# Kernel optimization log

Hardware: AMD Instinct MI355X
Metric: run time of the kernel (lower is better)

## Reference

```python
import jax, jax.numpy as jnp
import numpy as np

N, E = 100000, 1600000
ENT, OCU, SAI, IJ = 64, 64, 64, 8


def setup_inputs() -> dict:
    key = jax.random.key(0)
    ks = jax.random.split(key, 14)

    def lin(k, fan_in, fan_out):
        s = 1.0 / np.sqrt(fan_in)
        kw, kb = jax.random.split(k)
        w = jax.random.uniform(kw, (fan_in, fan_out), minval=-s, maxval=s, dtype=jnp.float32)
        b = jax.random.uniform(kb, (fan_out,), minval=-s, maxval=s, dtype=jnp.float32)
        return w, b

    we_w1, we_b1 = lin(ks[0], 2 * ENT + 1 + IJ, OCU)
    we_w2, we_b2 = lin(ks[1], OCU, OCU)
    wx_w1, wx_b1 = lin(ks[2], OCU, OCU)
    wx_w2, wx_b2 = lin(ks[3], OCU, 1)
    wh_w1, wh_b1 = lin(ks[4], ENT + OCU, OCU)
    wh_w2, wh_b2 = lin(ks[5], OCU, SAI)
    wv_w1, wv_b1 = lin(ks[6], ENT, OCU)
    wv_w2, wv_b2 = lin(ks[7], OCU, 1)

    return {
        "h": jax.random.normal(ks[8], (N, ENT), dtype=jnp.float32),
        "x": jax.random.normal(ks[9], (N, 3), dtype=jnp.float32),
        "velocidade": jax.random.normal(ks[10], (N, 3), dtype=jnp.float32),
        "atributos_arestas": jax.random.normal(ks[11], (E, IJ), dtype=jnp.float32),
        "we_w1": we_w1, "we_b1": we_b1, "we_w2": we_w2, "we_b2": we_b2,
        "wx_w1": wx_w1, "wx_b1": wx_b1, "wx_w2": wx_w2, "wx_b2": wx_b2,
        "wh_w1": wh_w1, "wh_b1": wh_b1, "wh_w2": wh_w2, "wh_b2": wh_b2,
        "wv_w1": wv_w1, "wv_b1": wv_b1, "wv_w2": wv_w2, "wv_b2": wv_b2,
        "arestas": jax.random.randint(ks[12], (2, E), 0, N, dtype=jnp.int32),
    }


def reference(h, x, velocidade, atributos_arestas,
              we_w1, we_b1, we_w2, we_b2,
              wx_w1, wx_b1, wx_w2, wx_b2,
              wh_w1, wh_b1, wh_w2, wh_b2,
              wv_w1, wv_b1, wv_w2, wv_b2,
              arestas):
    linhas, cols = arestas[0], arestas[1]
    n = h.shape[0]

    # gather endpoint coordinates, radial distance per edge
    diferenca = x[linhas] - x[cols]                            # [E, 3]
    dif_radial = jnp.sum(diferenca * diferenca, axis=1, keepdims=True)  # [E, 1]

    # edge MLP phi_e on [h_i, h_j, ||x_i-x_j||^2, edge_attr]
    atributos = jnp.concatenate([h[linhas], h[cols], dif_radial, atributos_arestas], axis=1)
    m_ij = jnp.tanh(jnp.tanh(atributos @ we_w1 + we_b1) @ we_w2 + we_b2)   # [E, OCU]

    # phi_x: per-edge scalar gate on coordinate differences
    phi_x = jnp.tanh(jnp.tanh(m_ij @ wx_w1 + wx_b1) @ wx_w2 + wx_b2)       # [E, 1]

    # phi_v: per-node scalar gate on velocity
    phi_v = jnp.tanh(h @ wv_w1 + wv_b1) @ wv_w2 + wv_b2                    # [N, 1]

    # segment-mean of (diferenca * phi_x) over source nodes
    trans = diferenca * phi_x                                              # [E, 3]
    agg_sum = jax.ops.segment_sum(trans, linhas, num_segments=n)           # [N, 3]
    cnt = jax.ops.segment_sum(jnp.ones((E, 1), trans.dtype), linhas, num_segments=n)
    agg_mean = agg_sum / jnp.maximum(cnt, 1.0)

    velocidade_nova = velocidade * phi_v + agg_mean
    x_nova = x + velocidade_nova

    # segment-sum of edge messages, node update phi_h
    m_i = jax.ops.segment_sum(m_ij, linhas, num_segments=n)                # [N, OCU]
    h_cat = jnp.concatenate([h, m_i], axis=1)
    h_nova = jnp.tanh(h_cat @ wh_w1 + wh_b1) @ wh_w2 + wh_b2               # [N, SAI]

    return (h_nova, x_nova, velocidade_nova)
```

## Files before the change

### kernel.cpp

```cpp
#include <hip/hip_runtime.h>


typedef unsigned int uint;
typedef unsigned short u16;
typedef __attribute__((ext_vector_type(8))) short short8;
typedef __attribute__((ext_vector_type(4))) float f32x4;

#define UB_LO(u) __uint_as_float((u) << 16)
#define UB_HI(u) __uint_as_float((u) & 0xffff0000u)

__device__ __forceinline__ float fast_tanh(float x) {
    float e = __expf(2.0f * x);
    return 1.0f - 2.0f * __builtin_amdgcn_rcpf(e + 1.0f);
}
__device__ __forceinline__ u16 bf16rne(float f) {
    uint u = __float_as_uint(f);
    return (u16)((u + 0x7fffu + ((u >> 16) & 1u)) >> 16);
}
__device__ __forceinline__ uint packbf(float a, float b) {
    return (uint)bf16rne(a) | ((uint)bf16rne(b) << 16);
}
__device__ __forceinline__ uint packbf_fast(float a, float b) {
    return __builtin_amdgcn_perm(__float_as_uint(b), __float_as_uint(a), 0x07060302u);
}
__device__ __forceinline__ u16 trunc16(float f) {
    return (u16)(__float_as_uint(f) >> 16);
}
__device__ __forceinline__ int swzb(int b) { return b ^ ((b >> 3) & 0x70); }

__global__ void wprep_hist_kernel(const float* __restrict__ we_w1, const float* __restrict__ we_w2,
                                  const float* __restrict__ wx_w1, const float* __restrict__ wv_w1,
                                  const float* __restrict__ wh_w1, const float* __restrict__ wh_w2,
                                  u16* __restrict__ we1t, u16* __restrict__ we2t,
                                  u16* __restrict__ wx1t, u16* __restrict__ wv1t,
                                  u16* __restrict__ wh1t, u16* __restrict__ wh2t,
                                  u16* __restrict__ wert,
                                  const int* __restrict__ rows, int* __restrict__ hist, int E) {
    const int b = blockIdx.x;
    if (b < 32) {
        int t = b * 256 + threadIdx.x;
        if (t < 8192) {
            int j = t >> 7, k = t & 127;
            we1t[t] = bf16rne(we_w1[k * 64 + j]);
            wh1t[t] = bf16rne(wh_w1[k * 64 + j]);
        }
        if (t < 4096) {
            int n = t >> 6, k = t & 63;
            we2t[t] = bf16rne(we_w2[k * 64 + n]);
            wx1t[t] = bf16rne(wx_w1[k * 64 + n]);
            wv1t[t] = bf16rne(wv_w1[k * 64 + n]);
            wh2t[t] = bf16rne(wh_w2[k * 64 + n]);
        }
        if (t < 2048) {
            int n = t >> 5, k = t & 31;
            float v = 0.0f;
            if (k == 0) v = we_w1[128 * 64 + n];
            else if (k <= 8) v = we_w1[(128 + k) * 64 + n];
            wert[t] = bf16rne(v);
        }
    } else {
        int e = (b - 32) * 256 + threadIdx.x;
        if (e < E) atomicAdd(&hist[rows[e]], 1);
    }
}

__global__ __launch_bounds__(256, 4)
void pre_mfma_kernel(const float* __restrict__ h, const float* __restrict__ we_b1,
                     const u16* __restrict__ we1t,
                     u16* __restrict__ HrB, u16* __restrict__ HcB, int N)
{
    __shared__ u16 X1[4096];
    __shared__ u16 X2[4096];
    const int tid = threadIdx.x, lane = tid & 63, wv = tid >> 6;
    const int nb = blockIdx.x * 64;
    const int el = tid >> 2, jg = tid & 3;
    const int fn = lane & 15, fk8 = (lane >> 4) * 8;

    {
        uint pk[8];
        if (nb + el < N) {
            const float4* h4 = (const float4*)(h + (size_t)(nb + el) * 64 + jg * 16);
            #pragma unroll
            for (int q = 0; q < 4; q++) {
                float4 v = h4[q];
                pk[2*q]   = packbf_fast(v.x, v.y);
                pk[2*q+1] = packbf_fast(v.z, v.w);
            }
        } else {
            #pragma unroll
            for (int q = 0; q < 8; q++) pk[q] = 0;
        }
        const int b0 = swzb(el * 128 + jg * 32), b1 = swzb(el * 128 + jg * 32 + 16);
        *(uint4*)(&X1[b0 >> 1]) = make_uint4(pk[0], pk[1], pk[2], pk[3]);
        *(uint4*)(&X1[b1 >> 1]) = make_uint4(pk[4], pk[5], pk[6], pk[7]);
    }
    __syncthreads();

    const int mb = wv * 16;
    short8 a0, a1;
    {
        const int ba = swzb((mb + fn) * 128 + fk8 * 2);
        const int bb = swzb((mb + fn) * 128 + 64 + fk8 * 2);
        a0 = *(const short8*)(&X1[ba >> 1]);
        a1 = *(const short8*)(&X1[bb >> 1]);
    }
    #pragma unroll
    for (int n0 = 0; n0 < 4; n0++) {
        uint4 bw0 = *(const uint4*)(we1t + (n0*16 + fn) * 128 + fk8);
        uint4 bw1 = *(const uint4*)(we1t + (n0*16 + fn) * 128 + 32 + fk8);
        const float bias = we_b1[n0 * 16 + fn];
        f32x4 q = {bias, bias, bias, bias};
        q = __builtin_amdgcn_mfma_f32_16x16x32_bf16(a0, __builtin_bit_cast(short8, bw0), q, 0, 0, 0);
        q = __builtin_amdgcn_mfma_f32_16x16x32_bf16(a1, __builtin_bit_cast(short8, bw1), q, 0, 0, 0);
        #pragma unroll
        for (int r2 = 0; r2 < 4; r2++) {
            const int m = mb + (lane >> 4) * 4 + r2;
            X2[swzb(m * 128 + (n0*16 + fn) * 2) >> 1] = bf16rne(q[r2]);
        }
    }
    __syncthreads();
    if (nb + el < N) {
        const int b0 = swzb(el * 128 + jg * 32), b1 = swzb(el * 128 + jg * 32 + 16);
        uint4 v0 = *(const uint4*)(&X2[b0 >> 1]);
        uint4 v1 = *(const uint4*)(&X2[b1 >> 1]);
        u16* o = HrB + (size_t)(nb + el) * 64 + jg * 16;
        *(uint4*)o = v0; *(uint4*)(o + 8) = v1;
    }
    __syncthreads();
    #pragma unroll
    for (int n0 = 0; n0 < 4; n0++) {
        uint4 bw0 = *(const uint4*)(we1t + (n0*16 + fn) * 128 + 64 + fk8);
        uint4 bw1 = *(const uint4*)(we1t + (n0*16 + fn) * 128 + 96 + fk8);
        f32x4 q = {0.f, 0.f, 0.f, 0.f};
        q = __builtin_amdgcn_mfma_f32_16x16x32_bf16(a0, __builtin_bit_cast(short8, bw0), q, 0, 0, 0);
        q = __builtin_amdgcn_mfma_f32_16x16x32_bf16(a1, __builtin_bit_cast(short8, bw1), q, 0, 0, 0);
        #pragma unroll
        for (int r2 = 0; r2 < 4; r2++) {
            const int m = mb + (lane >> 4) * 4 + r2;
            X2[swzb(m * 128 + (n0*16 + fn) * 2) >> 1] = bf16rne(q[r2]);
        }
    }
    __syncthreads();
    if (nb + el < N) {
        const int b0 = swzb(el * 128 + jg * 32), b1 = swzb(el * 128 + jg * 32 + 16);
        uint4 v0 = *(const uint4*)(&X2[b0 >> 1]);
        uint4 v1 = *(const uint4*)(&X2[b1 >> 1]);
        u16* o = HcB + (size_t)(nb + el) * 64 + jg * 16;
        *(uint4*)o = v0; *(uint4*)(o + 8) = v1;
    }
}

__global__ __launch_bounds__(256, 8)
void edge_mfma_kernel(const float* __restrict__ x, const float* __restrict__ eattr,
                      const uint4* __restrict__ rec4,
                      const u16* __restrict__ HrB, const u16* __restrict__ HcB,
                      const u16* __restrict__ wert,
                      const u16* __restrict__ we2t, const float* __restrict__ we_b2,
                      const u16* __restrict__ wx1t, const float* __restrict__ wx_b1,
                      const float* __restrict__ wx_w2, const float* __restrict__ wx_b2,
                      float* __restrict__ miF, float* __restrict__ aggF,
                      float* __restrict__ cntF, int E)
{
    __shared__ u16 T[4096];
    __shared__ float dS[64][3];
    __shared__ float pxS[64];
    __shared__ float radS[64];
    __shared__ int rS[64];
    __shared__ int eS[64];

    const int tid = threadIdx.x, lane = tid & 63, wv = tid >> 6;
    int bid = blockIdx.x;
    const int nwg = gridDim.x;
    if ((nwg & 7) == 0) bid = (bid & 7) * (nwg >> 3) + (bid >> 3);
    const int sb = bid * 64;
    const int fn = lane & 15, fk8 = (lane >> 4) * 8;
    const int el = tid >> 2, jg = tid & 3;
    const int s = sb + el;
    const int mb = wv * 16;

    {
        int r = -1, c = 0;
        if (s < E) { uint4 p4 = rec4[s]; r = (int)p4.x; c = (int)p4.y;
                     if (jg == 0) eS[el] = (int)p4.z; }
        if (jg == 0) rS[el] = r;
        uint pk[8];
        if (s < E) {
            if (jg == 0) {
                const float d0 = x[(size_t)r*3+0] - x[(size_t)c*3+0];
                const float d1 = x[(size_t)r*3+1] - x[(size_t)c*3+1];
                const float d2 = x[(size_t)r*3+2] - x[(size_t)c*3+2];
                dS[el][0] = d0; dS[el][1] = d1; dS[el][2] = d2;
                radS[el] = d0*d0 + d1*d1 + d2*d2;
            }
            uint4 ra = *(const uint4*)(HrB + (size_t)r * 64 + jg * 16);
            uint4 rb = *(const uint4*)(HrB + (size_t)r * 64 + jg * 16 + 8);
            uint4 ca = *(const uint4*)(HcB + (size_t)c * 64 + jg * 16);
            uint4 cb = *(const uint4*)(HcB + (size_t)c * 64 + jg * 16 + 8);
            uint rw[8] = {ra.x, ra.y, ra.z, ra.w, rb.x, rb.y, rb.z, rb.w};
            uint cw[8] = {ca.x, ca.y, ca.z, ca.w, cb.x, cb.y, cb.z, cb.w};
            #pragma unroll
            for (int q = 0; q < 8; q++) {
                const float lo = UB_LO(rw[q]) + UB_LO(cw[q]);
                const float hi = UB_HI(rw[q]) + UB_HI(cw[q]);
                pk[q] = packbf_fast(lo, hi);
            }
        } else {
            #pragma unroll
            for (int q = 0; q < 8; q++) pk[q] = 0;
        }
        const int b0 = swzb(el * 128 + jg * 32), b1 = swzb(el * 128 + jg * 32 + 16);
        *(uint4*)(&T[b0 >> 1]) = make_uint4(pk[0], pk[1], pk[2], pk[3]);
        *(uint4*)(&T[b1 >> 1]) = make_uint4(pk[4], pk[5], pk[6], pk[7]);
    }
    __syncthreads();

    uint ae[4] = {0, 0, 0, 0};
    {
        const int kc = lane >> 4;
        const int s2 = sb + mb + fn;
        if (kc < 2 && s2 < E) {
            const int e2 = eS[mb + fn];
            const float4* ea4 = (const float4*)(eattr + (size_t)e2 * 8);
            if (kc == 0) {
                float4 u0 = ea4[0], u1 = ea4[1];
                const float rad = radS[mb + fn];
                ae[0] = packbf_fast(rad,  u0.x);
                ae[1] = packbf_fast(u0.y, u0.z);
                ae[2] = packbf_fast(u0.w, u1.x);
                ae[3] = packbf_fast(u1.y, u1.z);
            } else {
                float4 u1 = ea4[1];
                ae[0] = packbf_fast(u1.w, 0.0f);
            }
        }
    }
    const short8 a_e = __builtin_bit_cast(short8, *(uint4*)ae);

    #pragma unroll
    for (int n0 = 0; n0 < 4; n0++) {
        uint4 bw = *(const uint4*)(wert + (n0*16 + fn) * 32 + fk8);
        f32x4 q = {0.f, 0.f, 0.f, 0.f};
        q = __builtin_amdgcn_mfma_f32_16x16x32_bf16(a_e, __builtin_bit_cast(short8, bw), q, 0, 0, 0);
        #pragma unroll
        for (int r2 = 0; r2 < 4; r2++) {
            const int idx = swzb((mb + (lane >> 4) * 4 + r2) * 128 + (n0*16 + fn) * 2) >> 1;
            const float pre = q[r2] + UB_LO((uint)T[idx]);
            T[idx] = trunc16(fast_tanh(pre));
        }
    }

    short8 a0, a1;
    {
        const int ba = swzb((mb + fn) * 128 + fk8 * 2);
        const int bb = swzb((mb + fn) * 128 + 64 + fk8 * 2);
        a0 = *(const short8*)(&T[ba >> 1]);
        a1 = *(const short8*)(&T[bb >> 1]);
    }
    #pragma unroll
    for (int n0 = 0; n0 < 4; n0++) {
        uint4 bw0 = *(const uint4*)(we2t + (n0*16 + fn) * 64 + fk8);
        uint4 bw1 = *(const uint4*)(we2t + (n0*16 + fn) * 64 + 32 + fk8);
        const float bias = we_b2[n0 * 16 + fn];
        f32x4 q = {bias, bias, bias, bias};
        q = __builtin_amdgcn_mfma_f32_16x16x32_bf16(a0, __builtin_bit_cast(short8, bw0), q, 0, 0, 0);
        q = __builtin_amdgcn_mfma_f32_16x16x32_bf16(a1, __builtin_bit_cast(short8, bw1), q, 0, 0, 0);
        #pragma unroll
        for (int r2 = 0; r2 < 4; r2++) {
            const int m = mb + (lane >> 4) * 4 + r2;
            T[swzb(m * 128 + (n0*16 + fn) * 2) >> 1] = bf16rne(fast_tanh(q[r2]));
        }
    }

    short8 c0, c1;
    {
        const int ba = swzb((mb + fn) * 128 + fk8 * 2);
        const int bb = swzb((mb + fn) * 128 + 64 + fk8 * 2);
        c0 = *(const short8*)(&T[ba >> 1]);
        c1 = *(const short8*)(&T[bb >> 1]);
    }
    float pxp[4] = {0.f, 0.f, 0.f, 0.f};
    #pragma unroll
    for (int n0 = 0; n0 < 4; n0++) {
        uint4 bw0 = *(const uint4*)(wx1t + (n0*16 + fn) * 64 + fk8);
        uint4 bw1 = *(const uint4*)(wx1t + (n0*16 + fn) * 64 + 32 + fk8);
        const float bias = wx_b1[n0 * 16 + fn];
        f32x4 q = {bias, bias, bias, bias};
        q = __builtin_amdgcn_mfma_f32_16x16x32_bf16(c0, __builtin_bit_cast(short8, bw0), q, 0, 0, 0);
        q = __builtin_amdgcn_mfma_f32_16x16x32_bf16(c1, __builtin_bit_cast(short8, bw1), q, 0, 0, 0);
        const float wqn = wx_w2[n0 * 16 + fn];
        #pragma unroll
        for (int r2 = 0; r2 < 4; r2++) pxp[r2] += fast_tanh(q[r2]) * wqn;
    }
    #pragma unroll
    for (int off = 1; off < 16; off <<= 1) {
        #pragma unroll
        for (int r2 = 0; r2 < 4; r2++) pxp[r2] += __shfl_xor(pxp[r2], off, 64);
    }
    if (fn == 0) {
        const float bx2 = wx_b2[0];
        #pragma unroll
        for (int r2 = 0; r2 < 4; r2++) {
            const int m = mb + (lane >> 4) * 4 + r2;
            pxS[m] = fast_tanh(pxp[r2] + bx2);
        }
    }
    __syncthreads();

    {
        const int rl = rS[lane];
        const int rp = (lane > 0) ? rS[lane - 1] : -2;
        const unsigned long long startm = __ballot(lane == 0 || rl != rp);
        unsigned long long m = startm & (0xFFFFull << (wv * 16));
        while (m) {
            const int s0 = (int)__builtin_ctzll(m);
            m &= m - 1;
            const int r0 = rS[s0];
            if (r0 < 0) continue;
            const unsigned long long rest = (startm >> s0) >> 1;
            const int s1 = rest ? s0 + 1 + (int)__builtin_ctzll(rest) : 64;
            float msum = 0.0f, tsum = 0.0f;
            for (int t = s0; t < s1; t++) {
                msum += UB_LO((uint)T[swzb(t * 128 + lane * 2) >> 1]);
                if (lane < 3) tsum += dS[t][lane] * pxS[t];
            }
            atomicAdd(&miF[(size_t)r0 * 64 + lane], msum);
            if (lane < 3) atomicAdd(&aggF[(size_t)r0 * 3 + lane], tsum);
            if (lane == 3) atomicAdd(&cntF[r0], (float)(s1 - s0));
        }
    }
}

__global__ __launch_bounds__(256, 4)
void aggnode_kernel(const float* __restrict__ h, const float* __restrict__ x,
                    const float* __restrict__ vel,
                    const float* __restrict__ miF, const float* __restrict__ aggF,
                    const float* __restrict__ cntF,
                    const u16* __restrict__ wv1t, const float* __restrict__ wv_b1,
                    const float* __restrict__ wv_w2, const float* __restrict__ wv_b2,
                    const u16* __restrict__ wh1t, const float* __restrict__ wh_b1,
                    const u16* __restrict__ wh2t, const float* __restrict__ wh_b2,
                    float* __restrict__ out_h, float* __restrict__ out_x,
                    float* __restrict__ out_v, int N)
{
    __shared__ u16 Xh[4096];
    __shared__ u16 Xm[4096];
    __shared__ float aggM[64][3];
    __shared__ float pvS[64];

    const int tid = threadIdx.x, lane = tid & 63, wv = tid >> 6;
    const int nb = blockIdx.x * 64;
    const int el = tid >> 2, jg = tid & 3;
    const int fn = lane & 15, fk8 = (lane >> 4) * 8;

    {
        uint pk[8];
        if (nb + el < N) {
            const float4* h4 = (const float4*)(h + (size_t)(nb + el) * 64 + jg * 16);
            #pragma unroll
            for (int q = 0; q < 4; q++) {
                float4 v = h4[q];
                pk[2*q]   = packbf_fast(v.x, v.y);
                pk[2*q+1] = packbf_fast(v.z, v.w);
            }
        } else {
            #pragma unroll
            for (int q = 0; q < 8; q++) pk[q] = 0;
        }
        const int b0 = swzb(el * 128 + jg * 32), b1 = swzb(el * 128 + jg * 32 + 16);
        *(uint4*)(&Xh[b0 >> 1]) = make_uint4(pk[0], pk[1], pk[2], pk[3]);
        *(uint4*)(&Xh[b1 >> 1]) = make_uint4(pk[4], pk[5], pk[6], pk[7]);
    }

    for (int t = 0; t < 16; t++) {
        const int ln = wv * 16 + t;
        const int n = nb + ln;
        float val = 0.0f;
        if (n < N) val = miF[(size_t)n * 64 + lane];
        Xm[swzb(ln * 128 + lane * 2) >> 1] = bf16rne(val);
        if (lane < 3 && n < N) {
            const float cf = cntF[n];
            aggM[ln][lane] = aggF[(size_t)n * 3 + lane] / fmaxf(cf, 1.0f);
        }
    }
    __syncthreads();

    const int mb = wv * 16;
    short8 a0, a1, b0, b1;
    {
        const int ba = swzb((mb + fn) * 128 + fk8 * 2);
        const int bb = swzb((mb + fn) * 128 + 64 + fk8 * 2);
        a0 = *(const short8*)(&Xh[ba >> 1]);
        a1 = *(const short8*)(&Xh[bb >> 1]);
        b0 = *(const short8*)(&Xm[ba >> 1]);
        b1 = *(const short8*)(&Xm[bb >> 1]);
    }

    float pvp[4] = {0.f, 0.f, 0.f, 0.f};
    #pragma unroll
    for (int n0 = 0; n0 < 4; n0++) {
        uint4 bw0 = *(const uint4*)(wv1t + (n0*16 + fn) * 64 + fk8);
        uint4 bw1 = *(const uint4*)(wv1t + (n0*16 + fn) * 64 + 32 + fk8);
        const float bias = wv_b1[n0 * 16 + fn];
        f32x4 q = {bias, bias, bias, bias};
        q = __builtin_amdgcn_mfma_f32_16x16x32_bf16(a0, __builtin_bit_cast(short8, bw0), q, 0, 0, 0);
        q = __builtin_amdgcn_mfma_f32_16x16x32_bf16(a1, __builtin_bit_cast(short8, bw1), q, 0, 0, 0);
        const float wqn = wv_w2[n0 * 16 + fn];
        #pragma unroll
        for (int r2 = 0; r2 < 4; r2++) pvp[r2] += fast_tanh(q[r2]) * wqn;
    }
    #pragma unroll
    for (int off = 1; off < 16; off <<= 1) {
        #pragma unroll
        for (int r2 = 0; r2 < 4; r2++) pvp[r2] += __shfl_xor(pvp[r2], off, 64);
    }
    if (fn == 0) {
        const float bv2 = wv_b2[0];
        #pragma unroll
        for (int r2 = 0; r2 < 4; r2++) pvS[mb + (lane >> 4) * 4 + r2] = pvp[r2] + bv2;
    }
    __syncthreads();

    #pragma unroll
    for (int n0 = 0; n0 < 4; n0++) {
        const u16* base = wh1t + (n0*16 + fn) * 128;
        uint4 bw0 = *(const uint4*)(base + fk8);
        uint4 bw1 = *(const uint4*)(base + 32 + fk8);
        uint4 bw2 = *(const uint4*)(base + 64 + fk8);
        uint4 bw3 = *(const uint4*)(base + 96 + fk8);
        const float bias = wh_b1[n0 * 16 + fn];
        f32x4 q = {bias, bias, bias, bias};
        q = __builtin_amdgcn_mfma_f32_16x16x32_bf16(a0, __builtin_bit_cast(short8, bw0), q, 0, 0, 0);
        q = __builtin_amdgcn_mfma_f32_16x16x32_bf16(a1, __builtin_bit_cast(short8, bw1), q, 0, 0, 0);
        q = __builtin_amdgcn_mfma_f32_16x16x32_bf16(b0, __builtin_bit_cast(short8, bw2), q, 0, 0, 0);
        q = __builtin_amdgcn_mfma_f32_16x16x32_bf16(b1, __builtin_bit_cast(short8, bw3), q, 0, 0, 0);
        #pragma unroll
        for (int r2 = 0; r2 < 4; r2++) {
            const int m = mb + (lane >> 4) * 4 + r2;
            Xm[swzb(m * 128 + (n0*16 + fn) * 2) >> 1] = bf16rne(fast_tanh(q[r2]));
        }
    }
    __syncthreads();

    short8 c0, c1;
    {
        const int ba = swzb((mb + fn) * 128 + fk8 * 2);
        const int bb = swzb((mb + fn) * 128 + 64 + fk8 * 2);
        c0 = *(const short8*)(&Xm[ba >> 1]);
        c1 = *(const short8*)(&Xm[bb >> 1]);
    }
    #pragma unroll
    for (int n0 = 0; n0 < 4; n0++) {
        uint4 bw0 = *(const uint4*)(wh2t + (n0*16 + fn) * 64 + fk8);
        uint4 bw1 = *(const uint4*)(wh2t + (n0*16 + fn) * 64 + 32 + fk8);
        const float bias = wh_b2[n0 * 16 + fn];
        f32x4 q = {bias, bias, bias, bias};
        q = __builtin_amdgcn_mfma_f32_16x16x32_bf16(c0, __builtin_bit_cast(short8, bw0), q, 0, 0, 0);
        q = __builtin_amdgcn_mfma_f32_16x16x32_bf16(c1, __builtin_bit_cast(short8, bw1), q, 0, 0, 0);
        #pragma unroll
        for (int r2 = 0; r2 < 4; r2++) {
            const int m = mb + (lane >> 4) * 4 + r2;
            if (nb + m < N) out_h[(size_t)(nb + m) * 64 + n0 * 16 + fn] = q[r2];
        }
    }

    if (tid < 64 && nb + tid < N) {
        const int n = nb + tid;
        const float pv = pvS[tid];
        #pragma unroll
        for (int d = 0; d < 3; d++) {
            const float am = aggM[tid][d];
            const float vn = vel[(size_t)n * 3 + d] * pv + am;
            out_v[(size_t)n * 3 + d] = vn;
            out_x[(size_t)n * 3 + d] = x[(size_t)n * 3 + d] + vn;
        }
    }
}

__global__ __launch_bounds__(256)
void scan1_kernel(const int* __restrict__ hist, int* __restrict__ bsum, int N) {
    const int t = threadIdx.x, b = blockIdx.x;
    const int base = b * 1024 + t * 4;
    int s = 0;
    #pragma unroll
    for (int q = 0; q < 4; q++) s += (base + q < N) ? hist[base + q] : 0;
    #pragma unroll
    for (int off = 1; off < 64; off <<= 1) s += __shfl_xor(s, off, 64);
    __shared__ int ws[4];
    if ((t & 63) == 0) ws[t >> 6] = s;
    __syncthreads();
    if (t == 0) bsum[b] = ws[0] + ws[1] + ws[2] + ws[3];
}

__global__ __launch_bounds__(256)
void scan2_kernel(int* __restrict__ bsum, int nb) {
    __shared__ int buf[1024];
    const int t = threadIdx.x;
    for (int i = t; i < nb; i += 256) buf[i] = bsum[i];
    __syncthreads();
    if (t == 0) {
        int run = 0;
        for (int i = 0; i < nb; i++) { int v = buf[i]; buf[i] = run; run += v; }
    }
    __syncthreads();
    for (int i = t; i < nb; i += 256) bsum[i] = buf[i];
}

__global__ __launch_bounds__(256)
void scan3_kernel(const int* __restrict__ hist, const int* __restrict__ bbase,
                  int* __restrict__ offs, int* __restrict__ cursor, int N) {
    const int t = threadIdx.x, b = blockIdx.x;
    const int base = b * 1024 + t * 4;
    int v[4];
    #pragma unroll
    for (int q = 0; q < 4; q++) v[q] = (base + q < N) ? hist[base + q] : 0;
    const int s = v[0] + v[1] + v[2] + v[3];
    const int lane = t & 63, wid = t >> 6;
    int inc = s;
    #pragma unroll
    for (int off = 1; off < 64; off <<= 1) {
        int u = __shfl_up(inc, off, 64);
        if (lane >= off) inc += u;
    }
    __shared__ int wtot[4];
    if (lane == 63) wtot[wid] = inc;
    __syncthreads();
    int wbase = 0;
    #pragma unroll
    for (int wq = 0; wq < 3; wq++) if (wq < wid) wbase += wtot[wq];
    int run = bbase[b] + wbase + (inc - s);
    #pragma unroll
    for (int q = 0; q < 4; q++) {
        const int i = base + q;
        if (i < N) { cursor[i] = run; run += v[q]; offs[i + 1] = run; }
    }
    if (b == 0 && t == 0) offs[0] = 0;
}

__global__ void scatter_kernel(const int* __restrict__ rows, const int* __restrict__ cols,
                               int* __restrict__ cursor, uint4* __restrict__ rec4, int E) {
    int e = blockIdx.x * blockDim.x + threadIdx.x;
    if (e < E) {
        int r = rows[e];
        int p = atomicAdd(&cursor[r], 1);
        rec4[p] = make_uint4((uint)r, (uint)cols[e], (uint)e, 0u);
    }
}

template<int BLK>
__global__ __launch_bounds__(BLK)
void edge_atomic_kernel(const float* __restrict__ h, const float* __restrict__ x,
                 const float* __restrict__ eattr,
                 const int* __restrict__ rows, const int* __restrict__ cols,
                 const float* __restrict__ we_w1, const float* __restrict__ we_b1,
                 const float* __restrict__ we_w2, const float* __restrict__ we_b2,
                 const float* __restrict__ wx_w1, const float* __restrict__ wx_b1,
                 const float* __restrict__ wx_w2, const float* __restrict__ wx_b2,
                 float* __restrict__ agg, float* __restrict__ cnt, float* __restrict__ mi,
                 int E)
{
    __shared__ float act[64][BLK];
    const int tid = threadIdx.x;
    const int e = blockIdx.x * BLK + tid;
    if (e >= E) return;

    const int r = rows[e];
    const int c = cols[e];
    const float d0 = x[(size_t)r*3+0] - x[(size_t)c*3+0];
    const float d1 = x[(size_t)r*3+1] - x[(size_t)c*3+1];
    const float d2 = x[(size_t)r*3+2] - x[(size_t)c*3+2];
    const float rad = d0*d0 + d1*d1 + d2*d2;

    float A[64];
    #pragma unroll
    for (int j = 0; j < 64; j++) A[j] = we_b1[j];
    const float* hr = h + (size_t)r * 64;
    const float* hc = h + (size_t)c * 64;
    #pragma unroll 4
    for (int k = 0; k < 64; k++) {
        const float a0 = hr[k];
        const float a1 = hc[k];
        const float* w0 = we_w1 + k * 64;
        const float* w1 = we_w1 + (64 + k) * 64;
        #pragma unroll
        for (int j = 0; j < 64; j++) A[j] += a0 * w0[j] + a1 * w1[j];
    }
    {
        const float* w = we_w1 + 128 * 64;
        #pragma unroll
        for (int j = 0; j < 64; j++) A[j] += rad * w[j];
    }
    const float* ea = eattr + (size_t)e * 8;
    #pragma unroll
    for (int k = 0; k < 8; k++) {
        const float a = ea[k];
        const float* w = we_w1 + (129 + k) * 64;
        #pragma unroll
        for (int j = 0; j < 64; j++) A[j] += a * w[j];
    }
    #pragma unroll
    for (int j = 0; j < 64; j++) act[j][tid] = fast_tanh(A[j]);

    float B[64];
    #pragma unroll
    for (int j = 0; j < 64; j++) B[j] = we_b2[j];
    #pragma unroll 4
    for (int k = 0; k < 64; k++) {
        const float a = act[k][tid];
        const float* w = we_w2 + k * 64;
        #pragma unroll
        for (int j = 0; j < 64; j++) B[j] += a * w[j];
    }
    #pragma unroll
    for (int j = 0; j < 64; j++) act[j][tid] = fast_tanh(B[j]);

    #pragma unroll
    for (int j = 0; j < 64; j++) A[j] = wx_b1[j];
    #pragma unroll 4
    for (int k = 0; k < 64; k++) {
        const float a = act[k][tid];
        const float* w = wx_w1 + k * 64;
        #pragma unroll
        for (int j = 0; j < 64; j++) A[j] += a * w[j];
    }
    float px = wx_b2[0];
    #pragma unroll
    for (int j = 0; j < 64; j++) px += fast_tanh(A[j]) * wx_w2[j];
    px = fast_tanh(px);

    atomicAdd(&agg[(size_t)r*3+0], d0 * px);
    atomicAdd(&agg[(size_t)r*3+1], d1 * px);
    atomicAdd(&agg[(size_t)r*3+2], d2 * px);
    atomicAdd(&cnt[r], 1.0f);
    float* mir = mi + (size_t)r * 64;
    #pragma unroll
    for (int j = 0; j < 64; j++) atomicAdd(&mir[j], act[j][tid]);
}

template<int BLK>
__global__ __launch_bounds__(BLK, 2)
void node_fb_kernel(const float* __restrict__ h, const float* __restrict__ x,
                 const float* __restrict__ vel,
                 const float* __restrict__ wh_w1, const float* __restrict__ wh_b1,
                 const float* __restrict__ wh_w2, const float* __restrict__ wh_b2,
                 const float* __restrict__ wv_w1, const float* __restrict__ wv_b1,
                 const float* __restrict__ wv_w2, const float* __restrict__ wv_b2,
                 const float* __restrict__ agg, const float* __restrict__ cnt,
                 const float* __restrict__ mi,
                 float* __restrict__ out_h, float* __restrict__ out_x, float* __restrict__ out_v,
                 int N)
{
    const int n = blockIdx.x * BLK + threadIdx.x;
    if (n >= N) return;

    const float* hn = h + (size_t)n * 64;
    const float* mn = mi + (size_t)n * 64;

    float A[64];
    #pragma unroll
    for (int j = 0; j < 64; j++) A[j] = wv_b1[j];
    #pragma unroll
    for (int k = 0; k < 64; k++) {
        const float a = hn[k];
        const float* w = wv_w1 + k * 64;
        #pragma unroll
        for (int j = 0; j < 64; j++) A[j] += a * w[j];
    }
    float pv = wv_b2[0];
    #pragma unroll
    for (int j = 0; j < 64; j++) pv += fast_tanh(A[j]) * wv_w2[j];

    #pragma unroll
    for (int j = 0; j < 64; j++) A[j] = wh_b1[j];
    #pragma unroll
    for (int k = 0; k < 64; k++) {
        const float a0 = hn[k];
        const float a1 = mn[k];
        const float* w0 = wh_w1 + k * 64;
        const float* w1 = wh_w1 + (64 + k) * 64;
        #pragma unroll
        for (int j = 0; j < 64; j++) A[j] += a0 * w0[j] + a1 * w1[j];
    }
    #pragma unroll
    for (int j = 0; j < 64; j++) A[j] = fast_tanh(A[j]);

    float B[64];
    #pragma unroll
    for (int j = 0; j < 64; j++) B[j] = wh_b2[j];
    #pragma unroll
    for (int k = 0; k < 64; k++) {
        const float a = A[k];
        const float* w = wh_w2 + k * 64;
        #pragma unroll
        for (int j = 0; j < 64; j++) B[j] += a * w[j];
    }
    float* oh = out_h + (size_t)n * 64;
    #pragma unroll
    for (int j = 0; j < 64; j++) oh[j] = B[j];

    const float inv = 1.0f / fmaxf(cnt[n], 1.0f);
    #pragma unroll
    for (int d = 0; d < 3; d++) {
        const float am = agg[(size_t)n*3 + d] * inv;
        const float vn = vel[(size_t)n*3 + d] * pv + am;
        out_v[(size_t)n*3 + d] = vn;
        out_x[(size_t)n*3 + d] = x[(size_t)n*3 + d] + vn;
    }
}

extern "C" void kernel_launch(void* const* d_in, const int* in_sizes, int n_in,
                              void* d_out, int out_size, void* d_ws, size_t ws_size,
                              hipStream_t stream) {
    const float* h      = (const float*)d_in[0];
    const float* x      = (const float*)d_in[1];
    const float* vel    = (const float*)d_in[2];
    const float* eattr  = (const float*)d_in[3];
    const float* we_w1  = (const float*)d_in[4];
    const float* we_b1  = (const float*)d_in[5];
    const float* we_w2  = (const float*)d_in[6];
    const float* we_b2  = (const float*)d_in[7];
    const float* wx_w1  = (const float*)d_in[8];
    const float* wx_b1  = (const float*)d_in[9];
    const float* wx_w2  = (const float*)d_in[10];
    const float* wx_b2  = (const float*)d_in[11];
    const float* wh_w1  = (const float*)d_in[12];
    const float* wh_b1  = (const float*)d_in[13];
    const float* wh_w2  = (const float*)d_in[14];
    const float* wh_b2  = (const float*)d_in[15];
    const float* wv_w1  = (const float*)d_in[16];
    const float* wv_b1  = (const float*)d_in[17];
    const float* wv_w2  = (const float*)d_in[18];
    const float* wv_b2  = (const float*)d_in[19];
    const int*   ar     = (const int*)d_in[20];

    const int N = in_sizes[0] / 64;
    const int E = in_sizes[20] / 2;
    const int* rows = ar;
    const int* cols = ar + E;

    float* out_h = (float*)d_out;
    float* out_x = out_h + (size_t)N * 64;
    float* out_v = out_x + (size_t)N * 3;

    u16* HrB = (u16*)d_out;
    u16* HcB = HrB + (size_t)N * 64;

    const int nbScan = (N + 1023) / 1024;

    char* p = (char*)d_ws;
    float* miF  = (float*)p; p += (size_t)N * 64 * sizeof(float);
    float* aggF = (float*)p; p += (size_t)N * 3 * sizeof(float);
    float* cntF = (float*)p; p += (size_t)N * sizeof(float);
    int*  hist  = (int*)p;   p += (size_t)N * sizeof(int);
    const size_t zero_bytes = (size_t)(p - (char*)d_ws);
    int*  offs  = (int*)p;   p += (size_t)(N + 1) * sizeof(int);
    int*  cursor= (int*)p;   p += (size_t)N * sizeof(int);
    int*  bsum  = (int*)p;   p += (size_t)(nbScan > 0 ? nbScan : 1) * sizeof(int);
    p = (char*)(((uintptr_t)p + 15) & ~(uintptr_t)15);
    uint4* rec4 = (uint4*)p; p += (size_t)E * sizeof(uint4);
    p = (char*)(((uintptr_t)p + 63) & ~(uintptr_t)63);
    u16*  we1t = (u16*)p;   p += 64 * 128 * sizeof(u16);
    u16*  we2t = (u16*)p;   p += 64 * 64 * sizeof(u16);
    u16*  wx1t = (u16*)p;   p += 64 * 64 * sizeof(u16);
    u16*  wv1t = (u16*)p;   p += 64 * 64 * sizeof(u16);
    u16*  wh1t = (u16*)p;   p += 64 * 128 * sizeof(u16);
    u16*  wh2t = (u16*)p;   p += 64 * 64 * sizeof(u16);
    u16*  wert = (u16*)p;   p += 64 * 32 * sizeof(u16);
    const size_t needed = (size_t)(p - (char*)d_ws);

    if (ws_size >= needed && nbScan <= 1024) {
        hipMemsetAsync(d_ws, 0, zero_bytes, stream);
        wprep_hist_kernel<<<32 + (E + 255) / 256, 256, 0, stream>>>(
            we_w1, we_w2, wx_w1, wv_w1, wh_w1, wh_w2,
            we1t, we2t, wx1t, wv1t, wh1t, wh2t, wert, rows, hist, E);
        scan1_kernel<<<nbScan, 256, 0, stream>>>(hist, bsum, N);
        scan2_kernel<<<1, 256, 0, stream>>>(bsum, nbScan);
        scan3_kernel<<<nbScan, 256, 0, stream>>>(hist, bsum, offs, cursor, N);
        scatter_kernel<<<(E + 255) / 256, 256, 0, stream>>>(rows, cols, cursor, rec4, E);

        pre_mfma_kernel<<<(N + 63) / 64, 256, 0, stream>>>(h, we_b1, we1t, HrB, HcB, N);

        edge_mfma_kernel<<<(E + 63) / 64, 256, 0, stream>>>(
            x, eattr, rec4, HrB, HcB,
            wert, we2t, we_b2, wx1t, wx_b1, wx_w2, wx_b2,
            miF, aggF, cntF, E);

        aggnode_kernel<<<(N + 63) / 64, 256, 0, stream>>>(
            h, x, vel, miF, aggF, cntF,
            wv1t, wv_b1, wv_w2, wv_b2,
            wh1t, wh_b1, wh2t, wh_b2,
            out_h, out_x, out_v, N);
    } else {
        float* agg2 = (float*)d_ws;
        float* cnt2 = agg2 + (size_t)N * 3;
        float* mi2  = cnt2 + N;
        hipMemsetAsync(d_ws, 0, (size_t)N * 68 * sizeof(float), stream);

        edge_atomic_kernel<128><<<(E + 127) / 128, 128, 0, stream>>>(
            h, x, eattr, rows, cols,
            we_w1, we_b1, we_w2, we_b2,
            wx_w1, wx_b1, wx_w2, wx_b2,
            agg2, cnt2, mi2, E);

        node_fb_kernel<128><<<(N + 127) / 128, 128, 0, stream>>>(
            h, x, vel,
            wh_w1, wh_b1, wh_w2, wh_b2,
            wv_w1, wv_b1, wv_w2, wv_b2,
            agg2, cnt2, mi2, out_h, out_x, out_v, N);
    }
}
```

Before: 555.8 us.

## Make edge kernel persistent with register prefetch of next tile's gathers

The edge kernel now launches a fixed grid of up to 2048 blocks, and each block walks a contiguous range of 64-edge tiles. While the current tile runs its MFMA chain, the block loads the next tile's sorted edge record, coordinate differences and bf16 node-feature rows into registers. This overlaps gather latency with compute and amortizes block launch cost. In exchange it uses more registers under a launch bound of 8 blocks per CU, adds a third barrier per tile, and can leave blocks with uneven work.

```diff
diff --git a/kernel.cpp b/kernel.cpp
--- a/kernel.cpp
+++ b/kernel.cpp
@@ -159,7 +159,7 @@
                       const u16* __restrict__ wx1t, const float* __restrict__ wx_b1,
                       const float* __restrict__ wx_w2, const float* __restrict__ wx_b2,
                       float* __restrict__ miF, float* __restrict__ aggF,
-                      float* __restrict__ cntF, int E)
+                      float* __restrict__ cntF, int E, int ntiles)
 {
     __shared__ u16 T[4096];
     __shared__ float dS[64][3];
@@ -169,165 +169,187 @@
     __shared__ int eS[64];
 
     const int tid = threadIdx.x, lane = tid & 63, wv = tid >> 6;
+    const int nwg = gridDim.x;
     int bid = blockIdx.x;
-    const int nwg = gridDim.x;
     if ((nwg & 7) == 0) bid = (bid & 7) * (nwg >> 3) + (bid >> 3);
-    const int sb = bid * 64;
+    const int tpb = (ntiles + nwg - 1) / nwg;
+    const int tbeg = bid * tpb;
+    const int tend = (tbeg + tpb < ntiles) ? (tbeg + tpb) : ntiles;
+    if (tbeg >= tend) return;
+
     const int fn = lane & 15, fk8 = (lane >> 4) * 8;
     const int el = tid >> 2, jg = tid & 3;
-    const int s = sb + el;
     const int mb = wv * 16;
 
-    {
-        int r = -1, c = 0;
-        if (s < E) { uint4 p4 = rec4[s]; r = (int)p4.x; c = (int)p4.y;
-                     if (jg == 0) eS[el] = (int)p4.z; }
-        if (jg == 0) rS[el] = r;
-        uint pk[8];
-        if (s < E) {
-            if (jg == 0) {
-                const float d0 = x[(size_t)r*3+0] - x[(size_t)c*3+0];
-                const float d1 = x[(size_t)r*3+1] - x[(size_t)c*3+1];
-                const float d2 = x[(size_t)r*3+2] - x[(size_t)c*3+2];
-                dS[el][0] = d0; dS[el][1] = d1; dS[el][2] = d2;
-                radS[el] = d0*d0 + d1*d1 + d2*d2;
-            }
-            uint4 ra = *(const uint4*)(HrB + (size_t)r * 64 + jg * 16);
-            uint4 rb = *(const uint4*)(HrB + (size_t)r * 64 + jg * 16 + 8);
-            uint4 ca = *(const uint4*)(HcB + (size_t)c * 64 + jg * 16);
-            uint4 cb = *(const uint4*)(HcB + (size_t)c * 64 + jg * 16 + 8);
-            uint rw[8] = {ra.x, ra.y, ra.z, ra.w, rb.x, rb.y, rb.z, rb.w};
-            uint cw[8] = {ca.x, ca.y, ca.z, ca.w, cb.x, cb.y, cb.z, cb.w};
+    int pr = -1, pe = 0;
+    float pd0 = 0.f, pd1 = 0.f, pd2 = 0.f, prad = 0.f;
+    uint4 pra = {0,0,0,0}, prb = {0,0,0,0}, pca = {0,0,0,0}, pcb = {0,0,0,0};
+
+#define LOADSTATE(TILE) do {                                                   \
+    const int s_ = (TILE) * 64 + el;                                           \
+    pr = -1; pe = 0;                                                           \
+    pra = make_uint4(0,0,0,0); prb = pra; pca = pra; pcb = pra;                \
+    if (s_ < E) {                                                              \
+        uint4 p4_ = rec4[s_];                                                  \
+        pr = (int)p4_.x; const int pc_ = (int)p4_.y; pe = (int)p4_.z;          \
+        if (jg == 0) {                                                         \
+            pd0 = x[(size_t)pr*3+0] - x[(size_t)pc_*3+0];                      \
+            pd1 = x[(size_t)pr*3+1] - x[(size_t)pc_*3+1];                      \
+            pd2 = x[(size_t)pr*3+2] - x[(size_t)pc_*3+2];                      \
+            prad = pd0*pd0 + pd1*pd1 + pd2*pd2;                                \
+        }                                                                      \
+        pra = *(const uint4*)(HrB + (size_t)pr * 64 + jg * 16);                \
+        prb = *(const uint4*)(HrB + (size_t)pr * 64 + jg * 16 + 8);            \
+        pca = *(const uint4*)(HcB + (size_t)pc_ * 64 + jg * 16);               \
+        pcb = *(const uint4*)(HcB + (size_t)pc_ * 64 + jg * 16 + 8);           \
+    }                                                                          \
+} while (0)
+
+    LOADSTATE(tbeg);
+
+    for (int tile = tbeg; tile < tend; tile++) {
+        const int sb = tile * 64;
+
+        if (jg == 0) {
+            rS[el] = pr; eS[el] = pe;
+            dS[el][0] = pd0; dS[el][1] = pd1; dS[el][2] = pd2;
+            radS[el] = prad;
+        }
+        {
+            uint rw[8] = {pra.x, pra.y, pra.z, pra.w, prb.x, prb.y, prb.z, prb.w};
+            uint cw[8] = {pca.x, pca.y, pca.z, pca.w, pcb.x, pcb.y, pcb.z, pcb.w};
+            uint pk[8];
             #pragma unroll
             for (int q = 0; q < 8; q++) {
                 const float lo = UB_LO(rw[q]) + UB_LO(cw[q]);
                 const float hi = UB_HI(rw[q]) + UB_HI(cw[q]);
                 pk[q] = packbf_fast(lo, hi);
             }
-        } else {
-            #pragma unroll
-            for (int q = 0; q < 8; q++) pk[q] = 0;
-        }
-        const int b0 = swzb(el * 128 + jg * 32), b1 = swzb(el * 128 + jg * 32 + 16);
-        *(uint4*)(&T[b0 >> 1]) = make_uint4(pk[0], pk[1], pk[2], pk[3]);
-        *(uint4*)(&T[b1 >> 1]) = make_uint4(pk[4], pk[5], pk[6], pk[7]);
-    }
-    __syncthreads();
-
-    uint ae[4] = {0, 0, 0, 0};
-    {
-        const int kc = lane >> 4;
-        const int s2 = sb + mb + fn;
-        if (kc < 2 && s2 < E) {
-            const int e2 = eS[mb + fn];
-            const float4* ea4 = (const float4*)(eattr + (size_t)e2 * 8);
-            if (kc == 0) {
-                float4 u0 = ea4[0], u1 = ea4[1];
-                const float rad = radS[mb + fn];
-                ae[0] = packbf_fast(rad,  u0.x);
-                ae[1] = packbf_fast(u0.y, u0.z);
-                ae[2] = packbf_fast(u0.w, u1.x);
-                ae[3] = packbf_fast(u1.y, u1.z);
-            } else {
-                float4 u1 = ea4[1];
-                ae[0] = packbf_fast(u1.w, 0.0f);
+            const int b0 = swzb(el * 128 + jg * 32), b1 = swzb(el * 128 + jg * 32 + 16);
+            *(uint4*)(&T[b0 >> 1]) = make_uint4(pk[0], pk[1], pk[2], pk[3]);
+            *(uint4*)(&T[b1 >> 1]) = make_uint4(pk[4], pk[5], pk[6], pk[7]);
+        }
+        __syncthreads();
+
+        if (tile + 1 < tend) LOADSTATE(tile + 1);
+
+        uint ae[4] = {0, 0, 0, 0};
+        {
+            const int kc = lane >> 4;
+            const int s2 = sb + mb + fn;
+            if (kc < 2 && s2 < E) {
+                const int e2 = eS[mb + fn];
+                const float4* ea4 = (const float4*)(eattr + (size_t)e2 * 8);
+                if (kc == 0) {
+                    float4 u0 = ea4[0], u1 = ea4[1];
+                    const float rad = radS[mb + fn];
+                    ae[0] = packbf_fast(rad,  u0.x);
+                    ae[1] = packbf_fast(u0.y, u0.z);
+                    ae[2] = packbf_fast(u0.w, u1.x);
+                    ae[3] = packbf_fast(u1.y, u1.z);
+                } else {
+                    float4 u1 = ea4[1];
+                    ae[0] = packbf_fast(u1.w, 0.0f);
+                }
             }
         }
-    }
-    const short8 a_e = __builtin_bit_cast(short8, *(uint4*)ae);
-
-    #pragma unroll
-    for (int n0 = 0; n0 < 4; n0++) {
-        uint4 bw = *(const uint4*)(wert + (n0*16 + fn) * 32 + fk8);
-        f32x4 q = {0.f, 0.f, 0.f, 0.f};
-        q = __builtin_amdgcn_mfma_f32_16x16x32_bf16(a_e, __builtin_bit_cast(short8, bw), q, 0, 0, 0);
-        #pragma unroll
-        for (int r2 = 0; r2 < 4; r2++) {
-            const int idx = swzb((mb + (lane >> 4) * 4 + r2) * 128 + (n0*16 + fn) * 2) >> 1;
-            const float pre = q[r2] + UB_LO((uint)T[idx]);
-            T[idx] = trunc16(fast_tanh(pre));
-        }
-    }
-
-    short8 a0, a1;
-    {
-        const int ba = swzb((mb + fn) * 128 + fk8 * 2);
-        const int bb = swzb((mb + fn) * 128 + 64 + fk8 * 2);
-        a0 = *(const short8*)(&T[ba >> 1]);
-        a1 = *(const short8*)(&T[bb >> 1]);
-    }
-    #pragma unroll
-    for (int n0 = 0; n0 < 4; n0++) {
-        uint4 bw0 = *(const uint4*)(we2t + (n0*16 + fn) * 64 + fk8);
-        uint4 bw1 = *(const uint4*)(we2t + (n0*16 + fn) * 64 + 32 + fk8);
-        const float bias = we_b2[n0 * 16 + fn];
-        f32x4 q = {bias, bias, bias, bias};
-        q = __builtin_amdgcn_mfma_f32_16x16x32_bf16(a0, __builtin_bit_cast(short8, bw0), q, 0, 0, 0);
-        q = __builtin_amdgcn_mfma_f32_16x16x32_bf16(a1, __builtin_bit_cast(short8, bw1), q, 0, 0, 0);
-        #pragma unroll
-        for (int r2 = 0; r2 < 4; r2++) {
-            const int m = mb + (lane >> 4) * 4 + r2;
-            T[swzb(m * 128 + (n0*16 + fn) * 2) >> 1] = bf16rne(fast_tanh(q[r2]));
-        }
-    }
-
-    short8 c0, c1;
-    {
-        const int ba = swzb((mb + fn) * 128 + fk8 * 2);
-        const int bb = swzb((mb + fn) * 128 + 64 + fk8 * 2);
-        c0 = *(const short8*)(&T[ba >> 1]);
-        c1 = *(const short8*)(&T[bb >> 1]);
-    }
-    float pxp[4] = {0.f, 0.f, 0.f, 0.f};
-    #pragma unroll
-    for (int n0 = 0; n0 < 4; n0++) {
-        uint4 bw0 = *(const uint4*)(wx1t + (n0*16 + fn) * 64 + fk8);
-        uint4 bw1 = *(const uint4*)(wx1t + (n0*16 + fn) * 64 + 32 + fk8);
-        const float bias = wx_b1[n0 * 16 + fn];
-        f32x4 q = {bias, bias, bias, bias};
-        q = __builtin_amdgcn_mfma_f32_16x16x32_bf16(c0, __builtin_bit_cast(short8, bw0), q, 0, 0, 0);
-        q = __builtin_amdgcn_mfma_f32_16x16x32_bf16(c1, __builtin_bit_cast(short8, bw1), q, 0, 0, 0);
-        const float wqn = wx_w2[n0 * 16 + fn];
-        #pragma unroll
-        for (int r2 = 0; r2 < 4; r2++) pxp[r2] += fast_tanh(q[r2]) * wqn;
-    }
-    #pragma unroll
-    for (int off = 1; off < 16; off <<= 1) {
-        #pragma unroll
-        for (int r2 = 0; r2 < 4; r2++) pxp[r2] += __shfl_xor(pxp[r2], off, 64);
-    }
-    if (fn == 0) {
-        const float bx2 = wx_b2[0];
-        #pragma unroll
-        for (int r2 = 0; r2 < 4; r2++) {
-            const int m = mb + (lane >> 4) * 4 + r2;
-            pxS[m] = fast_tanh(pxp[r2] + bx2);
-        }
-    }
-    __syncthreads();
-
-    {
-        const int rl = rS[lane];
-        const int rp = (lane > 0) ? rS[lane - 1] : -2;
-        const unsigned long long startm = __ballot(lane == 0 || rl != rp);
-        unsigned long long m = startm & (0xFFFFull << (wv * 16));
-        while (m) {
-            const int s0 = (int)__builtin_ctzll(m);
-            m &= m - 1;
-            const int r0 = rS[s0];
-            if (r0 < 0) continue;
-            const unsigned long long rest = (startm >> s0) >> 1;
-            const int s1 = rest ? s0 + 1 + (int)__builtin_ctzll(rest) : 64;
-            float msum = 0.0f, tsum = 0.0f;
-            for (int t = s0; t < s1; t++) {
-                msum += UB_LO((uint)T[swzb(t * 128 + lane * 2) >> 1]);
-                if (lane < 3) tsum += dS[t][lane] * pxS[t];
+        const short8 a_e = __builtin_bit_cast(short8, *(uint4*)ae);
+
+        #pragma unroll
+        for (int n0 = 0; n0 < 4; n0++) {
+            uint4 bw = *(const uint4*)(wert + (n0*16 + fn) * 32 + fk8);
+            f32x4 q = {0.f, 0.f, 0.f, 0.f};
+            q = __builtin_amdgcn_mfma_f32_16x16x32_bf16(a_e, __builtin_bit_cast(short8, bw), q, 0, 0, 0);
+            #pragma unroll
+            for (int r2 = 0; r2 < 4; r2++) {
+                const int idx = swzb((mb + (lane >> 4) * 4 + r2) * 128 + (n0*16 + fn) * 2) >> 1;
+                const float pre = q[r2] + UB_LO((uint)T[idx]);
+                T[idx] = trunc16(fast_tanh(pre));
             }
-            atomicAdd(&miF[(size_t)r0 * 64 + lane], msum);
-            if (lane < 3) atomicAdd(&aggF[(size_t)r0 * 3 + lane], tsum);
-            if (lane == 3) atomicAdd(&cntF[r0], (float)(s1 - s0));
-        }
-    }
+        }
+
+        short8 a0, a1;
+        {
+            const int ba = swzb((mb + fn) * 128 + fk8 * 2);
+            const int bb = swzb((mb + fn) * 128 + 64 + fk8 * 2);
+            a0 = *(const short8*)(&T[ba >> 1]);
+            a1 = *(const short8*)(&T[bb >> 1]);
+        }
+        #pragma unroll
+        for (int n0 = 0; n0 < 4; n0++) {
+            uint4 bw0 = *(const uint4*)(we2t + (n0*16 + fn) * 64 + fk8);
+            uint4 bw1 = *(const uint4*)(we2t + (n0*16 + fn) * 64 + 32 + fk8);
+            const float bias = we_b2[n0 * 16 + fn];
+            f32x4 q = {bias, bias, bias, bias};
+            q = __builtin_amdgcn_mfma_f32_16x16x32_bf16(a0, __builtin_bit_cast(short8, bw0), q, 0, 0, 0);
+            q = __builtin_amdgcn_mfma_f32_16x16x32_bf16(a1, __builtin_bit_cast(short8, bw1), q, 0, 0, 0);
+            #pragma unroll
+            for (int r2 = 0; r2 < 4; r2++) {
+                const int m = mb + (lane >> 4) * 4 + r2;
+                T[swzb(m * 128 + (n0*16 + fn) * 2) >> 1] = bf16rne(fast_tanh(q[r2]));
+            }
+        }
+
+        short8 c0, c1;
+        {
+            const int ba = swzb((mb + fn) * 128 + fk8 * 2);
+            const int bb = swzb((mb + fn) * 128 + 64 + fk8 * 2);
+            c0 = *(const short8*)(&T[ba >> 1]);
+            c1 = *(const short8*)(&T[bb >> 1]);
+        }
+        float pxp[4] = {0.f, 0.f, 0.f, 0.f};
+        #pragma unroll
+        for (int n0 = 0; n0 < 4; n0++) {
+            uint4 bw0 = *(const uint4*)(wx1t + (n0*16 + fn) * 64 + fk8);
+            uint4 bw1 = *(const uint4*)(wx1t + (n0*16 + fn) * 64 + 32 + fk8);
+            const float bias = wx_b1[n0 * 16 + fn];
+            f32x4 q = {bias, bias, bias, bias};
+            q = __builtin_amdgcn_mfma_f32_16x16x32_bf16(c0, __builtin_bit_cast(short8, bw0), q, 0, 0, 0);
+            q = __builtin_amdgcn_mfma_f32_16x16x32_bf16(c1, __builtin_bit_cast(short8, bw1), q, 0, 0, 0);
+            const float wqn = wx_w2[n0 * 16 + fn];
+            #pragma unroll
+            for (int r2 = 0; r2 < 4; r2++) pxp[r2] += fast_tanh(q[r2]) * wqn;
+        }
+        #pragma unroll
+        for (int off = 1; off < 16; off <<= 1) {
+            #pragma unroll
+            for (int r2 = 0; r2 < 4; r2++) pxp[r2] += __shfl_xor(pxp[r2], off, 64);
+        }
+        if (fn == 0) {
+            const float bx2 = wx_b2[0];
+            #pragma unroll
+            for (int r2 = 0; r2 < 4; r2++) {
+                const int m = mb + (lane >> 4) * 4 + r2;
+                pxS[m] = fast_tanh(pxp[r2] + bx2);
+            }
+        }
+        __syncthreads();
+
+        {
+            const int rl = rS[lane];
+            const int rp = (lane > 0) ? rS[lane - 1] : -2;
+            const unsigned long long startm = __ballot(lane == 0 || rl != rp);
+            unsigned long long m = startm & (0xFFFFull << (wv * 16));
+            while (m) {
+                const int s0 = (int)__builtin_ctzll(m);
+                m &= m - 1;
+                const int r0 = rS[s0];
+                if (r0 < 0) continue;
+                const unsigned long long rest = (startm >> s0) >> 1;
+                const int s1 = rest ? s0 + 1 + (int)__builtin_ctzll(rest) : 64;
+                float msum = 0.0f, tsum = 0.0f;
+                for (int t = s0; t < s1; t++) {
+                    msum += UB_LO((uint)T[swzb(t * 128 + lane * 2) >> 1]);
+                    if (lane < 3) tsum += dS[t][lane] * pxS[t];
+                }
+                atomicAdd(&miF[(size_t)r0 * 64 + lane], msum);
+                if (lane < 3) atomicAdd(&aggF[(size_t)r0 * 3 + lane], tsum);
+                if (lane == 3) atomicAdd(&cntF[r0], (float)(s1 - s0));
+            }
+        }
+        __syncthreads();
+    }
+#undef LOADSTATE
 }
 
 __global__ __launch_bounds__(256, 4)
@@ -745,6 +767,9 @@
     u16* HcB = HrB + (size_t)N * 64;
 
     const int nbScan = (N + 1023) / 1024;
+    const int ntiles = (E + 63) / 64;
+    int nblk = 2048;
+    if (ntiles < nblk) nblk = ntiles;
 
     char* p = (char*)d_ws;
     float* miF  = (float*)p; p += (size_t)N * 64 * sizeof(float);
@@ -779,10 +804,10 @@
 
         pre_mfma_kernel<<<(N + 63) / 64, 256, 0, stream>>>(h, we_b1, we1t, HrB, HcB, N);
 
-        edge_mfma_kernel<<<(E + 63) / 64, 256, 0, stream>>>(
+        edge_mfma_kernel<<<nblk, 256, 0, stream>>>(
             x, eattr, rec4, HrB, HcB,
             wert, we2t, we_b2, wx1t, wx_b1, wx_w2, wx_b2,
-            miF, aggF, cntF, E);
+            miF, aggF, cntF, E, ntiles);
 
         aggnode_kernel<<<(N + 63) / 64, 256, 0, stream>>>(
             h, x, vel, miF, aggF, cntF,
```

Result: slower. 1.180 ms (+112.3%).
